# Optimization experiments

Measured on AMD Instinct MI355X. Metric: run time of the kernel, lower is better.

The kernel has to match this reference:

```python
import jax, jax.numpy as jnp
import numpy as np

B, CIN, CH, COUT = 16, 256, 256, 256
RES = 16
E = 32           # embed_dim
NEMB = 1024      # codebook size
NP = 128         # n_phylo_channels (ch - NP == NP)
L = 4            # n_phylolevels
K = 8            # attribute codes per level per kernel
KN = 32          # nonattribute codes per kernel (levels=1)
CP = L * K * E   # 1024 projected phylo channels
CN = KN * E      # 1024 projected nonattr channels
BETA = 0.25
EPS = 1e-5

def conv1x1(x, w, b):
    # x: [B,C,H,W], w: [O,C], b: [O]
    return jnp.einsum('oc,bchw->bohw', w, x) + b[None, :, None, None]

def layernorm_chw(x, w, b):
    # LayerNorm over (C,H,W) per sample, elementwise affine of shape [C,H,W]
    mu = jnp.mean(x, axis=(1, 2, 3), keepdims=True)
    var = jnp.var(x, axis=(1, 2, 3), keepdims=True)
    return (x - mu) * jax.lax.rsqrt(var + EPS) * w[None] + b[None]

def reshape_in(x, levels):
    # [B, E*levels*K', H, W] -> [B, E, K'*H*W, levels]
    Bb, C, H, W = x.shape
    Kp = C // (E * levels)
    x = x.reshape(Bb, E, levels, Kp, H * W)
    x = x.transpose(0, 1, 3, 4, 2)          # [B,E,K',HW,levels]
    return x.reshape(Bb, E, Kp * H * W, levels)

def reshape_out(x, levels):
    # [B, E, K'*HW, levels] -> [B, E*levels*K', RES, RES]
    Bb, Ee, N, Ll = x.shape
    Kp = N // (RES * RES)
    x = x.reshape(Bb, Ee, Kp, RES * RES, Ll)
    x = x.transpose(0, 1, 4, 2, 3)          # [B,E,levels,K',HW]
    return x.reshape(Bb, Ee * Ll * Kp, RES, RES)

def quantize(z, codebook):
    # z: [B, E, N, levels]; codebook: [NEMB, E]
    zp = z.transpose(0, 2, 3, 1)            # [B,N,levels,E]
    flat = zp.reshape(-1, E)
    d = (jnp.sum(flat * flat, axis=1, keepdims=True)
         - 2.0 * flat @ codebook.T
         + jnp.sum(codebook * codebook, axis=1)[None, :])
    idx = jnp.argmin(d, axis=1)
    zq = codebook[idx].reshape(zp.shape)
    sg = jax.lax.stop_gradient
    loss = jnp.mean((sg(zq) - zp) ** 2) + BETA * jnp.mean((zq - sg(zp)) ** 2)
    zq = zp + sg(zq - zp)                   # straight-through
    return zq.transpose(0, 3, 1, 2), loss

def setup_inputs() -> dict:
    key = jax.random.key(0)
    ks = jax.random.split(key, 20)
    s = 0.02
    inp = {
        'x': jax.random.normal(ks[0], (B, CIN, RES, RES), jnp.float32),
        'conv_in_w': jax.random.normal(ks[1], (CH, CIN), jnp.float32) * s,
        'conv_in_b': jnp.zeros((CH,), jnp.float32),
        'ln_p_w': jnp.ones((NP, RES, RES), jnp.float32),
        'ln_p_b': jnp.zeros((NP, RES, RES), jnp.float32),
        'wp_in': jax.random.normal(ks[2], (CP, NP), jnp.float32) * s,
        'bp_in': jnp.zeros((CP,), jnp.float32),
        'wp_out': jax.random.normal(ks[3], (NP, CP), jnp.float32) * s,
        'bp_out': jnp.zeros((NP,), jnp.float32),
        'ln_n_w': jnp.ones((CH - NP, RES, RES), jnp.float32),
        'ln_n_b': jnp.zeros((CH - NP, RES, RES), jnp.float32),
        'wn_in': jax.random.normal(ks[4], (CN, CH - NP), jnp.float32) * s,
        'bn_in': jnp.zeros((CN,), jnp.float32),
        'wn_out': jax.random.normal(ks[5], (CH - NP, CN), jnp.float32) * s,
        'bn_out': jnp.zeros((CH - NP,), jnp.float32),
        'codebook': jax.random.uniform(ks[6], (NEMB, E), jnp.float32,
                                       -1.0 / NEMB, 1.0 / NEMB),
        'conv_out_w': jax.random.normal(ks[7], (COUT, CH), jnp.float32) * s,
        'conv_out_b': jnp.zeros((COUT,), jnp.float32),
    }
    return inp

def reference(x, conv_in_w, conv_in_b, ln_p_w, ln_p_b, wp_in, bp_in,
              wp_out, bp_out, ln_n_w, ln_n_b, wn_in, bn_in, wn_out, bn_out,
              codebook, conv_out_w, conv_out_b):
    silu = jax.nn.silu
    h = conv1x1(silu(x), conv_in_w, conv_in_b)
    h_p, h_n = h[:, :NP], h[:, NP:]
    # phylo branch
    z_p = silu(conv1x1(layernorm_chw(silu(h_p), ln_p_w, ln_p_b), wp_in, bp_in))
    zq_p, loss_p = quantize(reshape_in(z_p, L), codebook)
    hout_p = silu(conv1x1(reshape_out(zq_p, L), wp_out, bp_out))
    # non-attribute branch (anticlassification path)
    z_n = silu(conv1x1(layernorm_chw(silu(h_n), ln_n_w, ln_n_b), wn_in, bn_in))
    zq_n, loss_n = quantize(reshape_in(z_n, 1), codebook)
    hout_n = silu(conv1x1(reshape_out(zq_n, 1), wn_out, bn_out))
    h_cat = jnp.concatenate([hout_p, hout_n], axis=1)
    out = conv1x1(silu(h_cat), conv_out_w, conv_out_b)
    return out, loss_p + loss_n, zq_p
```

## Files before the change

### kernel.cpp

```cpp
#include <hip/hip_runtime.h>
#include <hip/hip_bf16.h>


__device__ __forceinline__ float silu_rx(float x){ return x / (1.f + expf(-x)); }
__device__ __forceinline__ float b2f_rx(__hip_bfloat16 v){ return __bfloat162float(v); }
__device__ __forceinline__ float ldv_rx(const void* p, int i, int f32m){
  if (f32m) return ((const float*)p)[i];
  return b2f_rx(((const __hip_bfloat16*)p)[i]);
}

#define FLAGS_OFF 0
#define LOSS_OFF  4
#define STATS_OFF 8
#define CB32_OFF  128
#define CBN_OFF   32896
#define IDXP_OFF  33984
#define IDXN_OFF  165056
#define R2_OFF    296192
#define R3_OFF    820480
#define R1_OFF    1344768

__global__ __launch_bounds__(256) void detect_rx(const void* cbv, float* flags, float* lossacc){
  __shared__ int bad;
  if (threadIdx.x == 0) bad = 0;
  __syncthreads();
  const unsigned short* u = (const unsigned short*)cbv;
  int local = 0;
  for (int i = threadIdx.x; i < 32768; i += 256){
    unsigned e = (u[i] >> 7) & 0xFF;
    if (e >= 126) local = 1;
  }
  if (local) bad = 1;
  __syncthreads();
  if (threadIdx.x == 0){
    flags[0] = bad ? 1.f : 0.f;
    lossacc[0] = 0.f; lossacc[1] = 0.f;
  }
}

__global__ __launch_bounds__(256) void cbprep_rx(const void* cbv, const float* flags,
                                                 float* cb32, float* cbn){
  const int f32m = (flags[0] != 0.f);
  int j = blockIdx.x * 256 + threadIdx.x;
  if (j < 1024){
    float s = 0.f;
    for (int e = 0; e < 32; ++e){
      float v = ldv_rx(cbv, j*32 + e, f32m);
      cb32[j*32 + e] = v;
      s += v*v;
    }
    cbn[j] = s;
  }
}

template<int KCH, int INMODE, bool OUTSILU, bool ATOMIC, int LEVELS>
__global__ __launch_bounds__(256) void gemm2_rx(
    const float* __restrict__ inF, const float* __restrict__ inF2,
    const void* __restrict__ inV,
    const void* __restrict__ W, const void* __restrict__ biasO,
    const void* __restrict__ sbA, const void* __restrict__ sbB,
    const int* __restrict__ idxin, const float* __restrict__ cb32,
    float* __restrict__ outF, const float* __restrict__ flags,
    int KDIM, int OUTC)
{
  __shared__ float As[32][32];
  __shared__ float Bs[32][68];
  __shared__ int   IdxS[32][32];

  const int f32m = (flags[0] != 0.f);
  const int t  = threadIdx.x;
  const int q0 = blockIdx.x << 5;
  const int b  = q0 >> 8;
  const int p0 = q0 & 255;
  const int o0 = blockIdx.y << 6;
  const int k0base = blockIdx.z * KCH;
  const int tx = t & 15, ty = t >> 4;
  float acc[4][2] = {};

  const int sch = t >> 3, spx = (t & 7) << 2;

  if constexpr (INMODE == 3){
    #pragma unroll
    for (int j = 0; j < 4; ++j){
      const int p = p0 + spx + j;
      if constexpr (LEVELS == 4){
        const int l = sch >> 3, kp = sch & 7;
        IdxS[sch][spx + j] = idxin[b*8192 + (((kp << 8) + p) << 2) + l];
      } else {
        IdxS[sch][spx + j] = idxin[b*8192 + (sch << 8) + p];
      }
    }
    __syncthreads();
  }

  for (int kc = 0; kc < KCH; kc += 32){
    const int k0 = k0base + kc;
    if constexpr (INMODE == 0){
      const float4 v = *reinterpret_cast<const float4*>(
          &inF[((b*KDIM + k0 + sch) << 8) + p0 + spx]);
      *reinterpret_cast<float4*>(&As[sch][spx]) = v;
    } else if constexpr (INMODE == 2){
      if (f32m){
        const float* xf = (const float*)inV;
        float4 v = *reinterpret_cast<const float4*>(&xf[((b*KDIM + k0 + sch) << 8) + p0 + spx]);
        v.x = silu_rx(v.x); v.y = silu_rx(v.y); v.z = silu_rx(v.z); v.w = silu_rx(v.w);
        *reinterpret_cast<float4*>(&As[sch][spx]) = v;
      } else {
        const __hip_bfloat16* xb = (const __hip_bfloat16*)inV;
        const int off = ((b*KDIM + k0 + sch) << 8) + p0 + spx;
        #pragma unroll
        for (int j = 0; j < 4; ++j) As[sch][spx + j] = silu_rx(b2f_rx(xb[off + j]));
      }
    } else if constexpr (INMODE == 3){
      const int e = k0 >> 5;
      #pragma unroll
      for (int j = 0; j < 4; ++j)
        As[sch][spx + j] = cb32[((IdxS[sch][spx + j] & 1023) << 5) + e];
    } else {
      const float* src = (k0 < 128) ? inF : inF2;
      const void* sb   = (k0 < 128) ? sbA : sbB;
      const int kh = k0 & 127;
      const float bb = ldv_rx(sb, kh + sch, f32m);
      float4 v = *reinterpret_cast<const float4*>(&src[((b*128 + kh + sch) << 8) + p0 + spx]);
      v.x = silu_rx(v.x + bb); v.y = silu_rx(v.y + bb);
      v.z = silu_rx(v.z + bb); v.w = silu_rx(v.w + bb);
      *reinterpret_cast<float4*>(&As[sch][spx]) = v;
    }
    if (f32m){
      const float* Wf = (const float*)W;
      #pragma unroll
      for (int r = 0; r < 8; ++r){
        int ii = t + (r << 8); int oo = ii >> 5, cc = ii & 31;
        Bs[cc][oo] = Wf[(o0 + oo)*KDIM + k0 + cc];
      }
    } else {
      const __hip_bfloat16* Wb = (const __hip_bfloat16*)W;
      #pragma unroll
      for (int r = 0; r < 8; ++r){
        int ii = t + (r << 8); int oo = ii >> 5, cc = ii & 31;
        Bs[cc][oo] = b2f_rx(Wb[(o0 + oo)*KDIM + k0 + cc]);
      }
    }
    __syncthreads();
    #pragma unroll
    for (int kk = 0; kk < 32; ++kk){
      const float2 a = *reinterpret_cast<const float2*>(&As[kk][tx << 1]);
      const float4 w = *reinterpret_cast<const float4*>(&Bs[kk][ty << 2]);
      acc[0][0] += w.x*a.x; acc[0][1] += w.x*a.y;
      acc[1][0] += w.y*a.x; acc[1][1] += w.y*a.y;
      acc[2][0] += w.z*a.x; acc[2][1] += w.z*a.y;
      acc[3][0] += w.w*a.x; acc[3][1] += w.w*a.y;
    }
    __syncthreads();
  }
  #pragma unroll
  for (int i = 0; i < 4; ++i){
    const int o = o0 + (ty << 2) + i;
    const int base = ((b*OUTC + o) << 8) + p0 + (tx << 1);
    if constexpr (ATOMIC){
      atomicAdd(&outF[base + 0], acc[i][0]);
      atomicAdd(&outF[base + 1], acc[i][1]);
    } else {
      const float bb = ldv_rx(biasO, o, f32m);
      float v0 = acc[i][0] + bb, v1 = acc[i][1] + bb;
      if constexpr (OUTSILU){ v0 = silu_rx(v0); v1 = silu_rx(v1); }
      *reinterpret_cast<float2*>(&outF[base]) = make_float2(v0, v1);
    }
  }
}

__global__ __launch_bounds__(256) void stats_rx(const float* __restrict__ h, float* __restrict__ stats){
  const int b = blockIdx.x >> 1, half = blockIdx.x & 1;
  const float* base = h + ((b*256 + half*128) << 8);
  float s = 0.f, s2 = 0.f;
  for (int i = threadIdx.x; i < 32768; i += 256){
    float a = silu_rx(base[i]);
    s += a; s2 += a*a;
  }
  __shared__ float sh[2][256];
  sh[0][threadIdx.x] = s; sh[1][threadIdx.x] = s2;
  __syncthreads();
  for (int st = 128; st > 0; st >>= 1){
    if (threadIdx.x < st){
      sh[0][threadIdx.x] += sh[0][threadIdx.x + st];
      sh[1][threadIdx.x] += sh[1][threadIdx.x + st];
    }
    __syncthreads();
  }
  if (threadIdx.x == 0){
    float mu  = sh[0][0] * (1.f/32768.f);
    float var = sh[1][0] * (1.f/32768.f) - mu*mu;
    stats[half*32 + b]      = mu;
    stats[half*32 + 16 + b] = 1.f / sqrtf(var + 1e-5f);
  }
}

__global__ __launch_bounds__(256) void ln_rx(const float* __restrict__ h,
    const void* lwp, const void* lbp, const void* lwn, const void* lbn,
    const float* __restrict__ stats, const float* __restrict__ flags,
    float* __restrict__ lnp, float* __restrict__ lnn){
  const int f32m = (flags[0] != 0.f);
  int i = blockIdx.x * 256 + threadIdx.x;
  int b = i >> 16, c = (i >> 8) & 255, p = i & 255;
  float a = silu_rx(h[i]);
  if (c < 128){
    float v = (a - stats[b]) * stats[16 + b] * ldv_rx(lwp, (c << 8) + p, f32m) + ldv_rx(lbp, (c << 8) + p, f32m);
    lnp[((b*128 + c) << 8) + p] = v;
  } else {
    int cc = c - 128;
    float v = (a - stats[32 + b]) * stats[48 + b] * ldv_rx(lwn, (cc << 8) + p, f32m) + ldv_rx(lbn, (cc << 8) + p, f32m);
    lnn[((b*128 + cc) << 8) + p] = v;
  }
}

template<int LEVELS>
__global__ __launch_bounds__(256) void quant_rx(const float* __restrict__ z,
    const float* __restrict__ cb32, const float* __restrict__ cbn,
    int* __restrict__ idxout, float* __restrict__ lossacc){
  __shared__ float4 cbT[2056];
  __shared__ float  cbnS[1056];
  __shared__ float  red[256];

  const int tid = threadIdx.x;
  const int gid = blockIdx.x * 256 + tid;
  const int pt = gid & 7;
  const int vbase = gid >> 3;

  const int w = vbase & 8191;
  int p, cbase;
  if (LEVELS == 4){
    int l = w & 3, n = w >> 2;
    p = n & 255; cbase = (l << 3) + (n >> 8);
  } else {
    p = w & 255; cbase = w >> 8;
  }

  #pragma unroll
  for (int q = 0; q < 4; ++q){
    const int i = tid + (q << 8);
    cbnS[i + (i >> 5)] = cbn[i];
  }

  int blk[4];
  float4 zv[4][8];
  float zn[4];
  #pragma unroll
  for (int k = 0; k < 4; ++k){
    const int vid = vbase + (k << 15);
    blk[k] = vid >> 13;
    const int zoff = ((blk[k] << 10) + cbase) << 8;
    float zs = 0.f;
    #pragma unroll
    for (int e4 = 0; e4 < 8; ++e4){
      float4 a;
      a.x = z[zoff + (((e4<<2)+0) << 13) + p];
      a.y = z[zoff + (((e4<<2)+1) << 13) + p];
      a.z = z[zoff + (((e4<<2)+2) << 13) + p];
      a.w = z[zoff + (((e4<<2)+3) << 13) + p];
      zv[k][e4] = a;
      zs += a.x*a.x; zs += a.y*a.y; zs += a.z*a.z; zs += a.w*a.w;
    }
    zn[k] = zs;
  }

  float best[4] = {__builtin_inff(), __builtin_inff(), __builtin_inff(), __builtin_inff()};
  int bi[4] = {0, 0, 0, 0};

  const int jl0 = pt << 5;
  for (int t = 0; t < 4; ++t){
    __syncthreads();
    const float4* g4 = reinterpret_cast<const float4*>(cb32) + (t << 11);
    #pragma unroll
    for (int r = 0; r < 8; ++r){
      const int idx = tid + (r << 8);
      cbT[idx + (idx >> 8)] = g4[idx];
    }
    __syncthreads();

    #pragma unroll 2
    for (int i = 0; i < 32; ++i){
      const int jl = jl0 + i;
      const int j  = (t << 8) + jl;
      const float4* c = &cbT[(jl << 3) + (jl >> 5)];
      float dot0 = 0.f, dot1 = 0.f, dot2 = 0.f, dot3 = 0.f;
      #pragma unroll
      for (int e4 = 0; e4 < 8; ++e4){
        const float4 cc = c[e4];
        dot0 = fmaf(zv[0][e4].x, cc.x, dot0); dot1 = fmaf(zv[1][e4].x, cc.x, dot1);
        dot2 = fmaf(zv[2][e4].x, cc.x, dot2); dot3 = fmaf(zv[3][e4].x, cc.x, dot3);
        dot0 = fmaf(zv[0][e4].y, cc.y, dot0); dot1 = fmaf(zv[1][e4].y, cc.y, dot1);
        dot2 = fmaf(zv[2][e4].y, cc.y, dot2); dot3 = fmaf(zv[3][e4].y, cc.y, dot3);
        dot0 = fmaf(zv[0][e4].z, cc.z, dot0); dot1 = fmaf(zv[1][e4].z, cc.z, dot1);
        dot2 = fmaf(zv[2][e4].z, cc.z, dot2); dot3 = fmaf(zv[3][e4].z, cc.z, dot3);
        dot0 = fmaf(zv[0][e4].w, cc.w, dot0); dot1 = fmaf(zv[1][e4].w, cc.w, dot1);
        dot2 = fmaf(zv[2][e4].w, cc.w, dot2); dot3 = fmaf(zv[3][e4].w, cc.w, dot3);
      }
      const float cn = cbnS[j + (j >> 5)];
      const float d0 = (zn[0] - 2.f*dot0) + cn;
      const float d1 = (zn[1] - 2.f*dot1) + cn;
      const float d2 = (zn[2] - 2.f*dot2) + cn;
      const float d3 = (zn[3] - 2.f*dot3) + cn;
      if (d0 < best[0]){ best[0] = d0; bi[0] = j; }
      if (d1 < best[1]){ best[1] = d1; bi[1] = j; }
      if (d2 < best[2]){ best[2] = d2; bi[2] = j; }
      if (d3 < best[3]){ best[3] = d3; bi[3] = j; }
    }
  }

  #pragma unroll
  for (int k = 4; k > 0; k >>= 1){
    #pragma unroll
    for (int v = 0; v < 4; ++v){
      float od = __shfl_down(best[v], k); int oj = __shfl_down(bi[v], k);
      if (od < best[v] || (od == best[v] && oj < bi[v])){ best[v] = od; bi[v] = oj; }
    }
  }
  if (pt == 0){
    #pragma unroll
    for (int v = 0; v < 4; ++v) idxout[blk[v]*8192 + w] = bi[v];
  }
  red[tid] = (pt == 0) ? (best[0] + best[1] + best[2] + best[3]) : 0.f;
  __syncthreads();
  for (int st = 128; st > 0; st >>= 1){
    if (tid < st) red[tid] += red[tid + st];
    __syncthreads();
  }
  if (tid == 0) atomicAdd(lossacc, red[0]);
}

__global__ __launch_bounds__(256) void zqout_rx(const int* __restrict__ idxp,
    const float* __restrict__ cb32, float* __restrict__ out){
  int t = blockIdx.x * 256 + threadIdx.x;
  int l = t & 3, n = (t >> 2) & 2047, e = (t >> 13) & 31, b = t >> 18;
  int id = idxp[b*8192 + (n << 2) + l];
  out[t] = cb32[((id & 1023) << 5) + e];
}

__global__ __launch_bounds__(256) void zero_rx(float* __restrict__ p){
  p[blockIdx.x * 256 + threadIdx.x] = 0.f;
}

__global__ void loss_rx(const float* __restrict__ lossacc, float* __restrict__ out){
  if (threadIdx.x == 0 && blockIdx.x == 0)
    out[0] = 1.25f * (lossacc[0] + lossacc[1]) * (1.f/4194304.f);
}

extern "C" void kernel_launch(void* const* d_in, const int* in_sizes, int n_in,
                              void* d_out, int out_size, void* d_ws, size_t ws_size,
                              hipStream_t stream){
  (void)in_sizes; (void)n_in; (void)out_size; (void)ws_size;
  const void* x   = d_in[0];
  const void* ciw = d_in[1];
  const void* cib = d_in[2];
  const void* lwp = d_in[3];
  const void* lbp = d_in[4];
  const void* wpi = d_in[5];
  const void* bpi = d_in[6];
  const void* wpo = d_in[7];
  const void* bpo = d_in[8];
  const void* lwn = d_in[9];
  const void* lbn = d_in[10];
  const void* wni = d_in[11];
  const void* bni = d_in[12];
  const void* wno = d_in[13];
  const void* bno = d_in[14];
  const void* cbk = d_in[15];
  const void* cow = d_in[16];
  const void* cob = d_in[17];

  float* ws    = (float*)d_ws;
  float* flags = ws + FLAGS_OFF;
  float* loss  = ws + LOSS_OFF;
  float* stats = ws + STATS_OFF;
  float* cb32  = ws + CB32_OFF;
  float* cbn   = ws + CBN_OFF;
  int*   idxp  = (int*)(ws + IDXP_OFF);
  int*   idxn  = (int*)(ws + IDXN_OFF);
  float* R2    = ws + R2_OFF;
  float* R3    = ws + R3_OFF;
  float* R1    = ws + R1_OFF;

  float* outO = (float*)d_out;
  float* outL = outO + 1048576;
  float* outZ = outO + 1048577;
  float* zbuf = outO;

  detect_rx<<<1, 256, 0, stream>>>(cbk, flags, loss);
  cbprep_rx<<<4, 256, 0, stream>>>(cbk, flags, cb32, cbn);
  gemm2_rx<256,2,false,false,0><<<dim3(128,4), 256, 0, stream>>>(
      nullptr, nullptr, x, ciw, cib, nullptr, nullptr, nullptr, nullptr,
      R1, flags, 256, 256);
  stats_rx<<<32, 256, 0, stream>>>(R1, stats);
  ln_rx<<<4096, 256, 0, stream>>>(R1, lwp, lbp, lwn, lbn, stats, flags, R2, R3);
  gemm2_rx<128,0,true,false,0><<<dim3(128,16), 256, 0, stream>>>(
      R2, nullptr, nullptr, wpi, bpi, nullptr, nullptr, nullptr, nullptr,
      zbuf, flags, 128, 1024);
  quant_rx<4><<<1024, 256, 0, stream>>>(zbuf, cb32, cbn, idxp, loss + 0);
  gemm2_rx<128,0,true,false,0><<<dim3(128,16), 256, 0, stream>>>(
      R3, nullptr, nullptr, wni, bni, nullptr, nullptr, nullptr, nullptr,
      zbuf, flags, 128, 1024);
  quant_rx<1><<<1024, 256, 0, stream>>>(zbuf, cb32, cbn, idxn, loss + 1);
  zqout_rx<<<16384, 256, 0, stream>>>(idxp, cb32, outZ);
  zero_rx<<<4096, 256, 0, stream>>>(R2);
  gemm2_rx<256,3,false,true,4><<<dim3(128,2,4), 256, 0, stream>>>(
      nullptr, nullptr, nullptr, wpo, nullptr, nullptr, nullptr, idxp, cb32,
      R2, flags, 1024, 128);
  gemm2_rx<256,3,false,true,1><<<dim3(128,2,4), 256, 0, stream>>>(
      nullptr, nullptr, nullptr, wno, nullptr, nullptr, nullptr, idxn, cb32,
      R3, flags, 1024, 128);
  gemm2_rx<256,5,false,false,0><<<dim3(128,4), 256, 0, stream>>>(
      R2, R3, nullptr, cow, cob, bpo, bno, nullptr, nullptr,
      outO, flags, 256, 256);
  loss_rx<<<1, 64, 0, stream>>>(loss, outL);
}
```

Baseline: 637.9 us.

## Simplify quantize to one vector per thread reading codebook from global

```diff
diff --git a/kernel.cpp b/kernel.cpp
--- a/kernel.cpp
+++ b/kernel.cpp
@@ -2,11 +2,11 @@
 #include <hip/hip_bf16.h>
 
 
-__device__ __forceinline__ float silu_rx(float x){ return x / (1.f + expf(-x)); }
-__device__ __forceinline__ float b2f_rx(__hip_bfloat16 v){ return __bfloat162float(v); }
-__device__ __forceinline__ float ldv_rx(const void* p, int i, int f32m){
+__device__ __forceinline__ float silu_ry(float x){ return x / (1.f + expf(-x)); }
+__device__ __forceinline__ float b2f_ry(__hip_bfloat16 v){ return __bfloat162float(v); }
+__device__ __forceinline__ float ldv_ry(const void* p, int i, int f32m){
   if (f32m) return ((const float*)p)[i];
-  return b2f_rx(((const __hip_bfloat16*)p)[i]);
+  return b2f_ry(((const __hip_bfloat16*)p)[i]);
 }
 
 #define FLAGS_OFF 0
@@ -20,7 +20,7 @@
 #define R3_OFF    820480
 #define R1_OFF    1344768
 
-__global__ __launch_bounds__(256) void detect_rx(const void* cbv, float* flags, float* lossacc){
+__global__ __launch_bounds__(256) void detect_ry(const void* cbv, float* flags, float* lossacc){
   __shared__ int bad;
   if (threadIdx.x == 0) bad = 0;
   __syncthreads();
@@ -38,14 +38,14 @@
   }
 }
 
-__global__ __launch_bounds__(256) void cbprep_rx(const void* cbv, const float* flags,
+__global__ __launch_bounds__(256) void cbprep_ry(const void* cbv, const float* flags,
                                                  float* cb32, float* cbn){
   const int f32m = (flags[0] != 0.f);
   int j = blockIdx.x * 256 + threadIdx.x;
   if (j < 1024){
     float s = 0.f;
     for (int e = 0; e < 32; ++e){
-      float v = ldv_rx(cbv, j*32 + e, f32m);
+      float v = ldv_ry(cbv, j*32 + e, f32m);
       cb32[j*32 + e] = v;
       s += v*v;
     }
@@ -54,7 +54,7 @@
 }
 
 template<int KCH, int INMODE, bool OUTSILU, bool ATOMIC, int LEVELS>
-__global__ __launch_bounds__(256) void gemm2_rx(
+__global__ __launch_bounds__(256) void gemm2_ry(
     const float* __restrict__ inF, const float* __restrict__ inF2,
     const void* __restrict__ inV,
     const void* __restrict__ W, const void* __restrict__ biasO,
@@ -103,13 +103,13 @@
       if (f32m){
         const float* xf = (const float*)inV;
         float4 v = *reinterpret_cast<const float4*>(&xf[((b*KDIM + k0 + sch) << 8) + p0 + spx]);
-        v.x = silu_rx(v.x); v.y = silu_rx(v.y); v.z = silu_rx(v.z); v.w = silu_rx(v.w);
+        v.x = silu_ry(v.x); v.y = silu_ry(v.y); v.z = silu_ry(v.z); v.w = silu_ry(v.w);
         *reinterpret_cast<float4*>(&As[sch][spx]) = v;
       } else {
         const __hip_bfloat16* xb = (const __hip_bfloat16*)inV;
         const int off = ((b*KDIM + k0 + sch) << 8) + p0 + spx;
         #pragma unroll
-        for (int j = 0; j < 4; ++j) As[sch][spx + j] = silu_rx(b2f_rx(xb[off + j]));
+        for (int j = 0; j < 4; ++j) As[sch][spx + j] = silu_ry(b2f_ry(xb[off + j]));
       }
     } else if constexpr (INMODE == 3){
       const int e = k0 >> 5;
@@ -120,10 +120,10 @@
       const float* src = (k0 < 128) ? inF : inF2;
       const void* sb   = (k0 < 128) ? sbA : sbB;
       const int kh = k0 & 127;
-      const float bb = ldv_rx(sb, kh + sch, f32m);
+      const float bb = ldv_ry(sb, kh + sch, f32m);
       float4 v = *reinterpret_cast<const float4*>(&src[((b*128 + kh + sch) << 8) + p0 + spx]);
-      v.x = silu_rx(v.x + bb); v.y = silu_rx(v.y + bb);
-      v.z = silu_rx(v.z + bb); v.w = silu_rx(v.w + bb);
+      v.x = silu_ry(v.x + bb); v.y = silu_ry(v.y + bb);
+      v.z = silu_ry(v.z + bb); v.w = silu_ry(v.w + bb);
       *reinterpret_cast<float4*>(&As[sch][spx]) = v;
     }
     if (f32m){
@@ -138,7 +138,7 @@
       #pragma unroll
       for (int r = 0; r < 8; ++r){
         int ii = t + (r << 8); int oo = ii >> 5, cc = ii & 31;
-        Bs[cc][oo] = b2f_rx(Wb[(o0 + oo)*KDIM + k0 + cc]);
+        Bs[cc][oo] = b2f_ry(Wb[(o0 + oo)*KDIM + k0 + cc]);
       }
     }
     __syncthreads();
@@ -161,20 +161,20 @@
       atomicAdd(&outF[base + 0], acc[i][0]);
       atomicAdd(&outF[base + 1], acc[i][1]);
     } else {
-      const float bb = ldv_rx(biasO, o, f32m);
+      const float bb = ldv_ry(biasO, o, f32m);
       float v0 = acc[i][0] + bb, v1 = acc[i][1] + bb;
-      if constexpr (OUTSILU){ v0 = silu_rx(v0); v1 = silu_rx(v1); }
+      if constexpr (OUTSILU){ v0 = silu_ry(v0); v1 = silu_ry(v1); }
       *reinterpret_cast<float2*>(&outF[base]) = make_float2(v0, v1);
     }
   }
 }
 
-__global__ __launch_bounds__(256) void stats_rx(const float* __restrict__ h, float* __restrict__ stats){
+__global__ __launch_bounds__(256) void stats_ry(const float* __restrict__ h, float* __restrict__ stats){
   const int b = blockIdx.x >> 1, half = blockIdx.x & 1;
   const float* base = h + ((b*256 + half*128) << 8);
   float s = 0.f, s2 = 0.f;
   for (int i = threadIdx.x; i < 32768; i += 256){
-    float a = silu_rx(base[i]);
+    float a = silu_ry(base[i]);
     s += a; s2 += a*a;
   }
   __shared__ float sh[2][256];
@@ -195,38 +195,31 @@
   }
 }
 
-__global__ __launch_bounds__(256) void ln_rx(const float* __restrict__ h,
+__global__ __launch_bounds__(256) void ln_ry(const float* __restrict__ h,
     const void* lwp, const void* lbp, const void* lwn, const void* lbn,
     const float* __restrict__ stats, const float* __restrict__ flags,
     float* __restrict__ lnp, float* __restrict__ lnn){
   const int f32m = (flags[0] != 0.f);
   int i = blockIdx.x * 256 + threadIdx.x;
   int b = i >> 16, c = (i >> 8) & 255, p = i & 255;
-  float a = silu_rx(h[i]);
+  float a = silu_ry(h[i]);
   if (c < 128){
-    float v = (a - stats[b]) * stats[16 + b] * ldv_rx(lwp, (c << 8) + p, f32m) + ldv_rx(lbp, (c << 8) + p, f32m);
+    float v = (a - stats[b]) * stats[16 + b] * ldv_ry(lwp, (c << 8) + p, f32m) + ldv_ry(lbp, (c << 8) + p, f32m);
     lnp[((b*128 + c) << 8) + p] = v;
   } else {
     int cc = c - 128;
-    float v = (a - stats[32 + b]) * stats[48 + b] * ldv_rx(lwn, (cc << 8) + p, f32m) + ldv_rx(lbn, (cc << 8) + p, f32m);
+    float v = (a - stats[32 + b]) * stats[48 + b] * ldv_ry(lwn, (cc << 8) + p, f32m) + ldv_ry(lbn, (cc << 8) + p, f32m);
     lnn[((b*128 + cc) << 8) + p] = v;
   }
 }
 
 template<int LEVELS>
-__global__ __launch_bounds__(256) void quant_rx(const float* __restrict__ z,
+__global__ __launch_bounds__(256) void quant_ry(const float* __restrict__ z,
     const float* __restrict__ cb32, const float* __restrict__ cbn,
     int* __restrict__ idxout, float* __restrict__ lossacc){
-  __shared__ float4 cbT[2056];
-  __shared__ float  cbnS[1056];
-  __shared__ float  red[256];
-
-  const int tid = threadIdx.x;
-  const int gid = blockIdx.x * 256 + tid;
-  const int pt = gid & 7;
-  const int vbase = gid >> 3;
-
-  const int w = vbase & 8191;
+  const int vid = blockIdx.x * 256 + threadIdx.x;
+  const int bl = vid >> 13;
+  const int w  = vid & 8191;
   int p, cbase;
   if (LEVELS == 4){
     int l = w & 3, n = w >> 2;
@@ -235,100 +228,43 @@
     p = w & 255; cbase = w >> 8;
   }
 
+  float zv[32]; float zn = 0.f;
+  const int zoff = ((bl << 10) + cbase) << 8;
   #pragma unroll
-  for (int q = 0; q < 4; ++q){
-    const int i = tid + (q << 8);
-    cbnS[i + (i >> 5)] = cbn[i];
-  }
-
-  int blk[4];
-  float4 zv[4][8];
-  float zn[4];
-  #pragma unroll
-  for (int k = 0; k < 4; ++k){
-    const int vid = vbase + (k << 15);
-    blk[k] = vid >> 13;
-    const int zoff = ((blk[k] << 10) + cbase) << 8;
-    float zs = 0.f;
+  for (int e = 0; e < 32; ++e){
+    float v = z[zoff + (e << 13) + p];
+    zv[e] = v; zn += v*v;
+  }
+
+  float best = __builtin_inff(); int bi = 0;
+  const float4* cb4 = reinterpret_cast<const float4*>(cb32);
+  #pragma unroll 2
+  for (int j = 0; j < 1024; ++j){
+    float dot = 0.f;
     #pragma unroll
     for (int e4 = 0; e4 < 8; ++e4){
-      float4 a;
-      a.x = z[zoff + (((e4<<2)+0) << 13) + p];
-      a.y = z[zoff + (((e4<<2)+1) << 13) + p];
-      a.z = z[zoff + (((e4<<2)+2) << 13) + p];
-      a.w = z[zoff + (((e4<<2)+3) << 13) + p];
-      zv[k][e4] = a;
-      zs += a.x*a.x; zs += a.y*a.y; zs += a.z*a.z; zs += a.w*a.w;
-    }
-    zn[k] = zs;
-  }
-
-  float best[4] = {__builtin_inff(), __builtin_inff(), __builtin_inff(), __builtin_inff()};
-  int bi[4] = {0, 0, 0, 0};
-
-  const int jl0 = pt << 5;
-  for (int t = 0; t < 4; ++t){
-    __syncthreads();
-    const float4* g4 = reinterpret_cast<const float4*>(cb32) + (t << 11);
-    #pragma unroll
-    for (int r = 0; r < 8; ++r){
-      const int idx = tid + (r << 8);
-      cbT[idx + (idx >> 8)] = g4[idx];
-    }
-    __syncthreads();
-
-    #pragma unroll 2
-    for (int i = 0; i < 32; ++i){
-      const int jl = jl0 + i;
-      const int j  = (t << 8) + jl;
-      const float4* c = &cbT[(jl << 3) + (jl >> 5)];
-      float dot0 = 0.f, dot1 = 0.f, dot2 = 0.f, dot3 = 0.f;
-      #pragma unroll
-      for (int e4 = 0; e4 < 8; ++e4){
-        const float4 cc = c[e4];
-        dot0 = fmaf(zv[0][e4].x, cc.x, dot0); dot1 = fmaf(zv[1][e4].x, cc.x, dot1);
-        dot2 = fmaf(zv[2][e4].x, cc.x, dot2); dot3 = fmaf(zv[3][e4].x, cc.x, dot3);
-        dot0 = fmaf(zv[0][e4].y, cc.y, dot0); dot1 = fmaf(zv[1][e4].y, cc.y, dot1);
-        dot2 = fmaf(zv[2][e4].y, cc.y, dot2); dot3 = fmaf(zv[3][e4].y, cc.y, dot3);
-        dot0 = fmaf(zv[0][e4].z, cc.z, dot0); dot1 = fmaf(zv[1][e4].z, cc.z, dot1);
-        dot2 = fmaf(zv[2][e4].z, cc.z, dot2); dot3 = fmaf(zv[3][e4].z, cc.z, dot3);
-        dot0 = fmaf(zv[0][e4].w, cc.w, dot0); dot1 = fmaf(zv[1][e4].w, cc.w, dot1);
-        dot2 = fmaf(zv[2][e4].w, cc.w, dot2); dot3 = fmaf(zv[3][e4].w, cc.w, dot3);
-      }
-      const float cn = cbnS[j + (j >> 5)];
-      const float d0 = (zn[0] - 2.f*dot0) + cn;
-      const float d1 = (zn[1] - 2.f*dot1) + cn;
-      const float d2 = (zn[2] - 2.f*dot2) + cn;
-      const float d3 = (zn[3] - 2.f*dot3) + cn;
-      if (d0 < best[0]){ best[0] = d0; bi[0] = j; }
-      if (d1 < best[1]){ best[1] = d1; bi[1] = j; }
-      if (d2 < best[2]){ best[2] = d2; bi[2] = j; }
-      if (d3 < best[3]){ best[3] = d3; bi[3] = j; }
-    }
-  }
-
-  #pragma unroll
-  for (int k = 4; k > 0; k >>= 1){
-    #pragma unroll
-    for (int v = 0; v < 4; ++v){
-      float od = __shfl_down(best[v], k); int oj = __shfl_down(bi[v], k);
-      if (od < best[v] || (od == best[v] && oj < bi[v])){ best[v] = od; bi[v] = oj; }
-    }
-  }
-  if (pt == 0){
-    #pragma unroll
-    for (int v = 0; v < 4; ++v) idxout[blk[v]*8192 + w] = bi[v];
-  }
-  red[tid] = (pt == 0) ? (best[0] + best[1] + best[2] + best[3]) : 0.f;
+      const float4 cc = cb4[(j << 3) + e4];
+      dot = fmaf(zv[(e4 << 2) + 0], cc.x, dot);
+      dot = fmaf(zv[(e4 << 2) + 1], cc.y, dot);
+      dot = fmaf(zv[(e4 << 2) + 2], cc.z, dot);
+      dot = fmaf(zv[(e4 << 2) + 3], cc.w, dot);
+    }
+    const float d = (zn - 2.f*dot) + cbn[j];
+    if (d < best){ best = d; bi = j; }
+  }
+
+  idxout[vid] = bi;
+  __shared__ float red[256];
+  red[threadIdx.x] = best;
   __syncthreads();
   for (int st = 128; st > 0; st >>= 1){
-    if (tid < st) red[tid] += red[tid + st];
-    __syncthreads();
-  }
-  if (tid == 0) atomicAdd(lossacc, red[0]);
-}
-
-__global__ __launch_bounds__(256) void zqout_rx(const int* __restrict__ idxp,
+    if (threadIdx.x < st) red[threadIdx.x] += red[threadIdx.x + st];
+    __syncthreads();
+  }
+  if (threadIdx.x == 0) atomicAdd(lossacc, red[0]);
+}
+
+__global__ __launch_bounds__(256) void zqout_ry(const int* __restrict__ idxp,
     const float* __restrict__ cb32, float* __restrict__ out){
   int t = blockIdx.x * 256 + threadIdx.x;
   int l = t & 3, n = (t >> 2) & 2047, e = (t >> 13) & 31, b = t >> 18;
@@ -336,11 +272,11 @@
   out[t] = cb32[((id & 1023) << 5) + e];
 }
 
-__global__ __launch_bounds__(256) void zero_rx(float* __restrict__ p){
+__global__ __launch_bounds__(256) void zero_ry(float* __restrict__ p){
   p[blockIdx.x * 256 + threadIdx.x] = 0.f;
 }
 
-__global__ void loss_rx(const float* __restrict__ lossacc, float* __restrict__ out){
+__global__ void loss_ry(const float* __restrict__ lossacc, float* __restrict__ out){
   if (threadIdx.x == 0 && blockIdx.x == 0)
     out[0] = 1.25f * (lossacc[0] + lossacc[1]) * (1.f/4194304.f);
 }
@@ -385,31 +321,31 @@
   float* outZ = outO + 1048577;
   float* zbuf = outO;
 
-  detect_rx<<<1, 256, 0, stream>>>(cbk, flags, loss);
-  cbprep_rx<<<4, 256, 0, stream>>>(cbk, flags, cb32, cbn);
-  gemm2_rx<256,2,false,false,0><<<dim3(128,4), 256, 0, stream>>>(
+  detect_ry<<<1, 256, 0, stream>>>(cbk, flags, loss);
+  cbprep_ry<<<4, 256, 0, stream>>>(cbk, flags, cb32, cbn);
+  gemm2_ry<256,2,false,false,0><<<dim3(128,4), 256, 0, stream>>>(
       nullptr, nullptr, x, ciw, cib, nullptr, nullptr, nullptr, nullptr,
       R1, flags, 256, 256);
-  stats_rx<<<32, 256, 0, stream>>>(R1, stats);
-  ln_rx<<<4096, 256, 0, stream>>>(R1, lwp, lbp, lwn, lbn, stats, flags, R2, R3);
-  gemm2_rx<128,0,true,false,0><<<dim3(128,16), 256, 0, stream>>>(
+  stats_ry<<<32, 256, 0, stream>>>(R1, stats);
+  ln_ry<<<4096, 256, 0, stream>>>(R1, lwp, lbp, lwn, lbn, stats, flags, R2, R3);
+  gemm2_ry<128,0,true,false,0><<<dim3(128,16), 256, 0, stream>>>(
       R2, nullptr, nullptr, wpi, bpi, nullptr, nullptr, nullptr, nullptr,
       zbuf, flags, 128, 1024);
-  quant_rx<4><<<1024, 256, 0, stream>>>(zbuf, cb32, cbn, idxp, loss + 0);
-  gemm2_rx<128,0,true,false,0><<<dim3(128,16), 256, 0, stream>>>(
+  quant_ry<4><<<512, 256, 0, stream>>>(zbuf, cb32, cbn, idxp, loss + 0);
+  gemm2_ry<128,0,true,false,0><<<dim3(128,16), 256, 0, stream>>>(
       R3, nullptr, nullptr, wni, bni, nullptr, nullptr, nullptr, nullptr,
       zbuf, flags, 128, 1024);
-  quant_rx<1><<<1024, 256, 0, stream>>>(zbuf, cb32, cbn, idxn, loss + 1);
-  zqout_rx<<<16384, 256, 0, stream>>>(idxp, cb32, outZ);
-  zero_rx<<<4096, 256, 0, stream>>>(R2);
-  gemm2_rx<256,3,false,true,4><<<dim3(128,2,4), 256, 0, stream>>>(
+  quant_ry<1><<<512, 256, 0, stream>>>(zbuf, cb32, cbn, idxn, loss + 1);
+  zqout_ry<<<16384, 256, 0, stream>>>(idxp, cb32, outZ);
+  zero_ry<<<4096, 256, 0, stream>>>(R2);
+  gemm2_ry<256,3,false,true,4><<<dim3(128,2,4), 256, 0, stream>>>(
       nullptr, nullptr, nullptr, wpo, nullptr, nullptr, nullptr, idxp, cb32,
       R2, flags, 1024, 128);
-  gemm2_rx<256,3,false,true,1><<<dim3(128,2,4), 256, 0, stream>>>(
+  gemm2_ry<256,3,false,true,1><<<dim3(128,2,4), 256, 0, stream>>>(
       nullptr, nullptr, nullptr, wno, nullptr, nullptr, nullptr, idxn, cb32,
       R3, flags, 1024, 128);
-  gemm2_rx<256,5,false,false,0><<<dim3(128,4), 256, 0, stream>>>(
+  gemm2_ry<256,5,false,false,0><<<dim3(128,4), 256, 0, stream>>>(
       R2, R3, nullptr, cow, cob, bpo, bno, nullptr, nullptr,
       outO, flags, 256, 256);
-  loss_rx<<<1, 64, 0, stream>>>(loss, outL);
-}
+  loss_ry<<<1, 64, 0, stream>>>(loss, outL);
+}
```

New measurement: 994.1 us. 1.56x slower.
